# Optimization experiments

Measured on AMD Instinct MI355X. Metric: run time of the kernel, lower is better.

The kernel has to match this reference:

```python
import jax, jax.numpy as jnp
import numpy as np


def gcn_conv(h, W, b, src, dst):
    # PyG GCNConv: h @ W, add self-loops, symmetric deg^-1/2 normalization,
    # scatter-add messages from src to dst, then add bias.
    n = h.shape[0]
    h = h @ W                                   # [N, out]
    loop = jnp.arange(n, dtype=src.dtype)
    row = jnp.concatenate([src, loop])          # message sources
    col = jnp.concatenate([dst, loop])          # aggregation targets
    deg = jax.ops.segment_sum(jnp.ones_like(col, dtype=h.dtype), col, num_segments=n)
    dinv = jnp.where(deg > 0, jax.lax.rsqrt(deg), 0.0)
    norm = dinv[row] * dinv[col]                # [E+N]
    out = jax.ops.segment_sum(h[row] * norm[:, None], col, num_segments=n)
    return out + b


def setup_inputs() -> dict:
    key = jax.random.key(0)
    ks = jax.random.split(key, 12)
    N, E = 50000, 800000
    in_dim, hid, out_dim = 768, 256, 128
    x = jax.random.normal(ks[0], (N, in_dim), dtype=jnp.float32)
    edge_index = jax.random.randint(ks[1], (2, E), 0, N, dtype=jnp.int64)

    def lin(k, fan_in, fan_out):
        bound = 1.0 / np.sqrt(fan_in)
        kw, kb = jax.random.split(k)
        W = jax.random.uniform(kw, (fan_in, fan_out), jnp.float32, -bound, bound)
        b = jax.random.uniform(kb, (fan_out,), jnp.float32, -bound, bound)
        return W, b

    W1, b1 = lin(ks[2], in_dim, hid)
    Wg1, bg1 = lin(ks[3], hid, hid)
    Wg2, bg2 = lin(ks[4], hid, hid)
    W2, b2 = lin(ks[5], hid, out_dim)
    Wc, bc = lin(ks[6], out_dim, 2)
    return {
        "x": x, "edge_index": edge_index,
        "W1": W1, "b1": b1, "Wg1": Wg1, "bg1": bg1,
        "Wg2": Wg2, "bg2": bg2, "W2": W2, "b2": b2,
        "Wc": Wc, "bc": bc, "batch_size": 1024,
    }


def reference(x, edge_index, W1, b1, Wg1, bg1, Wg2, bg2, W2, b2, Wc, bc, batch_size):
    src, dst = edge_index[0], edge_index[1]
    h = jax.nn.relu(x @ W1 + b1)                # linear_relu1
    h = gcn_conv(h, Wg1, bg1, src, dst)         # text1
    # dropout is identity in eval mode
    h = gcn_conv(h, Wg2, bg2, src, dst)         # text2
    h = jax.nn.relu(h @ W2 + b2)                # linear_relu2
    logits = h @ Wc + bc                        # classifier
    return logits[:batch_size]
```

## Files before the change

### kernel.cpp

```cpp
#include <hip/hip_runtime.h>
#include <hip/hip_bf16.h>
#include <cstdint>
#include <cstddef>
#include <type_traits>

typedef _Float16 half8 __attribute__((ext_vector_type(8)));
typedef _Float16 half4v __attribute__((ext_vector_type(4)));
typedef float float4v __attribute__((ext_vector_type(4)));


__global__ void k_zero_int(int* __restrict__ p, int n) {
  int i = blockIdx.x * blockDim.x + threadIdx.x;
  if (i < n) p[i] = 0;
}

__global__ void k_count(const int* __restrict__ dst, int* __restrict__ cnt, int E) {
  int e = blockIdx.x * blockDim.x + threadIdx.x;
  if (e < E) atomicAdd(&cnt[dst[e]], 1);
}

__global__ __launch_bounds__(1024) void k_scan_local(const int* __restrict__ cnt,
                                                     int* __restrict__ rowp,
                                                     int* __restrict__ bsum, int n) {
  __shared__ int sm[1024];
  int tid = threadIdx.x;
  int i = blockIdx.x * 1024 + tid;
  int v = (i < n) ? cnt[i] : 0;
  sm[tid] = v;
  __syncthreads();
  for (int off = 1; off < 1024; off <<= 1) {
    int t = (tid >= off) ? sm[tid - off] : 0;
    __syncthreads();
    sm[tid] += t;
    __syncthreads();
  }
  if (i < n) rowp[i] = sm[tid] - v;
  if (tid == 1023) bsum[blockIdx.x] = sm[1023];
}

__global__ __launch_bounds__(1024) void k_scan_sums(int* __restrict__ bsum, int nb) {
  __shared__ int sm[1024];
  int tid = threadIdx.x;
  int v = (tid < nb) ? bsum[tid] : 0;
  sm[tid] = v;
  __syncthreads();
  for (int off = 1; off < 1024; off <<= 1) {
    int t = (tid >= off) ? sm[tid - off] : 0;
    __syncthreads();
    sm[tid] += t;
    __syncthreads();
  }
  if (tid < nb) bsum[tid] = sm[tid] - v;
}

__global__ void k_finalize(int* __restrict__ rowp, const int* __restrict__ bsum,
                           const int* __restrict__ cnt, int* __restrict__ cursor,
                           float* __restrict__ dinv, int n, int E) {
  int i = blockIdx.x * blockDim.x + threadIdx.x;
  if (i < n) {
    int v = rowp[i] + bsum[i >> 10];
    rowp[i] = v;
    cursor[i] = v;
    dinv[i] = rsqrtf((float)(cnt[i] + 1));
  }
  if (i == 0) rowp[n] = E;
}

__global__ void k_fill(const int* __restrict__ src, const int* __restrict__ dst,
                       int* __restrict__ cursor, int* __restrict__ csr_src, int E) {
  int e = blockIdx.x * blockDim.x + threadIdx.x;
  if (e < E) {
    int pos = atomicAdd(&cursor[dst[e]], 1);
    csr_src[pos] = src[e];
  }
}


__global__ void k_w_convert_all(const float* __restrict__ W1, const float* __restrict__ Wg1,
                                const float* __restrict__ Wg2, _Float16* __restrict__ W1t,
                                _Float16* __restrict__ Wg1t, _Float16* __restrict__ Wg2t,
                                int in_dim, int hid) {
  int idx = blockIdx.x * blockDim.x + threadIdx.x;
  int n1 = in_dim * hid;
  int n2 = hid * hid;
  if (idx < n1) {
    int n = idx / in_dim, k = idx - n * in_dim;
    W1t[idx] = (_Float16)W1[(size_t)k * hid + n];
  } else if (idx < n1 + n2) {
    int i2 = idx - n1;
    int n = i2 / hid, k = i2 - n * hid;
    Wg1t[i2] = (_Float16)Wg1[(size_t)k * hid + n];
  } else if (idx < n1 + 2 * n2) {
    int i2 = idx - n1 - n2;
    int n = i2 / hid, k = i2 - n * hid;
    Wg2t[i2] = (_Float16)Wg2[(size_t)k * hid + n];
  }
}


#define LDSS 40

template <typename AT>
__device__ __forceinline__ half8 load_row_h8(const AT* __restrict__ p, bool ok) {
  half8 v = {};
  if (ok) {
    if constexpr (std::is_same_v<AT, float>) {
      float4 f0 = *(const float4*)p;
      float4 f1 = *(const float4*)(p + 4);
      v[0] = (_Float16)f0.x; v[1] = (_Float16)f0.y;
      v[2] = (_Float16)f0.z; v[3] = (_Float16)f0.w;
      v[4] = (_Float16)f1.x; v[5] = (_Float16)f1.y;
      v[6] = (_Float16)f1.z; v[7] = (_Float16)f1.w;
    } else {
      v = *(const half8*)p;
    }
  }
  return v;
}

template <typename AT, int RELU, int BIAS>
__global__ __launch_bounds__(256, 3) void k_gemm_mfma(const AT* __restrict__ A,
                                                      const _Float16* __restrict__ Bt,
                                                      const float* __restrict__ bias,
                                                      _Float16* __restrict__ out,
                                                      int M, int N, int K) {
  __shared__ _Float16 Asm[2][128 * LDSS];
  __shared__ _Float16 Bsm[2][128 * LDSS];
  const int tid = threadIdx.x;
  const int bm = blockIdx.y * 128;
  const int bn = blockIdx.x * 128;
  const int wave = tid >> 6;
  const int wm = (wave >> 1) * 64;
  const int wn = (wave & 1) * 64;
  const int quad = (tid & 63) >> 4;
  const int l15 = tid & 15;
  const int r0 = tid >> 2;
  const int c0 = (tid & 3) * 8;

  const int gr0 = bm + r0, gr1 = bm + r0 + 64;
  const bool ok0 = gr0 < M, ok1 = gr1 < M;
  const AT* Ap0 = A + (size_t)gr0 * K + c0;
  const AT* Ap1 = A + (size_t)gr1 * K + c0;
  const _Float16* Bp0 = Bt + (size_t)(bn + r0) * K + c0;
  const _Float16* Bp1 = Bt + (size_t)(bn + r0 + 64) * K + c0;

  _Float16* As0 = &Asm[0][0] + r0 * LDSS + c0;
  _Float16* As1 = &Asm[0][0] + (r0 + 64) * LDSS + c0;
  _Float16* Bs0 = &Bsm[0][0] + r0 * LDSS + c0;
  _Float16* Bs1 = &Bsm[0][0] + (r0 + 64) * LDSS + c0;
  const int bufstep = 128 * LDSS;

  float4v acc[4][4];
#pragma unroll
  for (int i = 0; i < 4; ++i)
#pragma unroll
    for (int j = 0; j < 4; ++j) acc[i][j] = (float4v){0.f, 0.f, 0.f, 0.f};

  half8 pa0 = load_row_h8<AT>(Ap0, ok0);
  half8 pa1 = load_row_h8<AT>(Ap1, ok1);
  half8 pb0 = *(const half8*)Bp0;
  half8 pb1 = *(const half8*)Bp1;
  *(half8*)As0 = pa0;
  *(half8*)As1 = pa1;
  *(half8*)Bs0 = pb0;
  *(half8*)Bs1 = pb1;

  const int nk = K >> 5;
  int buf = 0;
  for (int kt = 0; kt < nk; ++kt) {
    __syncthreads();
    if (kt + 1 < nk) {
      int k0 = (kt + 1) << 5;
      pa0 = load_row_h8<AT>(Ap0 + k0, ok0);
      pa1 = load_row_h8<AT>(Ap1 + k0, ok1);
      pb0 = *(const half8*)(Bp0 + k0);
      pb1 = *(const half8*)(Bp1 + k0);
    }
    const _Float16* Ab = &Asm[0][0] + buf * bufstep;
    const _Float16* Bb = &Bsm[0][0] + buf * bufstep;
    half8 af[4], bf[4];
#pragma unroll
    for (int i = 0; i < 4; ++i)
      af[i] = *(const half8*)(Ab + (wm + i * 16 + l15) * LDSS + quad * 8);
#pragma unroll
    for (int j = 0; j < 4; ++j)
      bf[j] = *(const half8*)(Bb + (wn + j * 16 + l15) * LDSS + quad * 8);
#pragma unroll
    for (int i = 0; i < 4; ++i)
#pragma unroll
      for (int j = 0; j < 4; ++j)
        acc[i][j] = __builtin_amdgcn_mfma_f32_16x16x32_f16(af[i], bf[j], acc[i][j], 0, 0, 0);
    if (kt + 1 < nk) {
      int nbuf = buf ^ 1;
      *(half8*)(As0 + nbuf * bufstep) = pa0;
      *(half8*)(As1 + nbuf * bufstep) = pa1;
      *(half8*)(Bs0 + nbuf * bufstep) = pb0;
      *(half8*)(Bs1 + nbuf * bufstep) = pb1;
    }
    buf ^= 1;
  }

#pragma unroll
  for (int j = 0; j < 4; ++j) {
    int c = bn + wn + j * 16 + l15;
    float bv = BIAS ? bias[c] : 0.f;
#pragma unroll
    for (int i = 0; i < 4; ++i) {
      int rbase = bm + wm + i * 16 + quad * 4;
      float4v a = acc[i][j];
#pragma unroll
      for (int reg = 0; reg < 4; ++reg) {
        int r = rbase + reg;
        if (r < M) {
          float v = a[reg] + bv;
          if (RELU) v = fmaxf(v, 0.f);
          out[(size_t)r * N + c] = (_Float16)v;
        }
      }
    }
  }
}


template <int RELU, int BIAS>
__global__ __launch_bounds__(256) void k_gemm(const float* __restrict__ A,
                                              const float* __restrict__ B,
                                              const float* __restrict__ bias,
                                              float* __restrict__ C,
                                              int M, int N, int K) {
  __shared__ float As[16][68];
  __shared__ float Bs[16][68];
  const int bm = blockIdx.y * 64;
  const int bn = blockIdx.x * 64;
  const int tid = threadIdx.x;
  const int tr = (tid >> 4) << 2;
  const int tc = (tid & 15) << 2;
  const int lm  = tid >> 2;
  const int lk  = (tid & 3) << 2;
  const int lk2 = tid >> 4;
  const int ln  = (tid & 15) << 2;
  const bool arow_ok = (bm + lm) < M;
  const float* Aptr = A + (size_t)(bm + lm) * K + lk;
  const float* Bptr = B + (size_t)lk2 * N + bn + ln;
  float acc[4][4] = {};
  for (int k0 = 0; k0 < K; k0 += 16) {
    float4 a4 = make_float4(0.f, 0.f, 0.f, 0.f);
    if (arow_ok) a4 = *(const float4*)(Aptr + k0);
    float4 b4 = *(const float4*)(Bptr + (size_t)k0 * N);
    As[lk + 0][lm] = a4.x;
    As[lk + 1][lm] = a4.y;
    As[lk + 2][lm] = a4.z;
    As[lk + 3][lm] = a4.w;
    *(float4*)&Bs[lk2][ln] = b4;
    __syncthreads();
#pragma unroll
    for (int k = 0; k < 16; ++k) {
      float4 av = *(const float4*)&As[k][tr];
      float4 bv = *(const float4*)&Bs[k][tc];
      float a[4] = {av.x, av.y, av.z, av.w};
      float b[4] = {bv.x, bv.y, bv.z, bv.w};
#pragma unroll
      for (int i = 0; i < 4; ++i)
#pragma unroll
        for (int j = 0; j < 4; ++j) acc[i][j] += a[i] * b[j];
    }
    __syncthreads();
  }
  float bias_v[4] = {0.f, 0.f, 0.f, 0.f};
  if (BIAS) {
    float4 bb = *(const float4*)(bias + bn + tc);
    bias_v[0] = bb.x; bias_v[1] = bb.y; bias_v[2] = bb.z; bias_v[3] = bb.w;
  }
#pragma unroll
  for (int i = 0; i < 4; ++i) {
    int r = bm + tr + i;
    if (r < M) {
      float4 o;
      o.x = acc[i][0] + bias_v[0];
      o.y = acc[i][1] + bias_v[1];
      o.z = acc[i][2] + bias_v[2];
      o.w = acc[i][3] + bias_v[3];
      if (RELU) {
        o.x = fmaxf(o.x, 0.f); o.y = fmaxf(o.y, 0.f);
        o.z = fmaxf(o.z, 0.f); o.w = fmaxf(o.w, 0.f);
      }
      *(float4*)&C[(size_t)r * N + bn + tc] = o;
    }
  }
}


template <typename OT>
__global__ __launch_bounds__(256) void k_agg(const _Float16* __restrict__ t,
                                             const int* __restrict__ row_ptr,
                                             const int* __restrict__ csr_src,
                                             const float* __restrict__ dinv,
                                             const float* __restrict__ bias,
                                             OT* __restrict__ out, int n_nodes) {
  int w = (int)((blockIdx.x * 256 + threadIdx.x) >> 6);
  int lane = threadIdx.x & 63;
  if (w >= n_nodes) return;
  float di = dinv[w];
  half4v v = *(const half4v*)(t + (size_t)w * 256 + lane * 4);
  float sw = di * di;
  float ax = (float)v[0] * sw, ay = (float)v[1] * sw, az = (float)v[2] * sw, aw = (float)v[3] * sw;
  int e0 = row_ptr[w], e1 = row_ptr[w + 1];
  for (int e = e0; e < e1; ++e) {
    int s = csr_src[e];
    float wgt = dinv[s] * di;
    half4v u = *(const half4v*)(t + (size_t)s * 256 + lane * 4);
    ax += (float)u[0] * wgt; ay += (float)u[1] * wgt;
    az += (float)u[2] * wgt; aw += (float)u[3] * wgt;
  }
  const float4 b = ((const float4*)bias)[lane];
  if constexpr (std::is_same_v<OT, float>) {
    float4 o;
    o.x = ax + b.x; o.y = ay + b.y; o.z = az + b.z; o.w = aw + b.w;
    ((float4*)(out + (size_t)w * 256))[lane] = o;
  } else {
    half4v o;
    o[0] = (_Float16)(ax + b.x); o[1] = (_Float16)(ay + b.y);
    o[2] = (_Float16)(az + b.z); o[3] = (_Float16)(aw + b.w);
    *(half4v*)(out + (size_t)w * 256 + lane * 4) = o;
  }
}


__global__ __launch_bounds__(256) void k_cls(const float* __restrict__ h,
                                             const float* __restrict__ Wc,
                                             const float* __restrict__ bc,
                                             float* __restrict__ out, int M, int K) {
  __shared__ float w[512];
  for (int i = threadIdx.x; i < 2 * K; i += 256) w[i] = Wc[i];
  __syncthreads();
  int i = blockIdx.x * 256 + threadIdx.x;
  if (i >= M) return;
  float a0 = bc[0], a1 = bc[1];
  const float* hr = h + (size_t)i * K;
  for (int k = 0; k < K; ++k) {
    float a = hr[k];
    a0 += a * w[2 * k];
    a1 += a * w[2 * k + 1];
  }
  out[2 * i] = a0;
  out[2 * i + 1] = a1;
}


extern "C" void kernel_launch(void* const* d_in, const int* in_sizes, int n_in,
                              void* d_out, int out_size, void* d_ws, size_t ws_size,
                              hipStream_t stream) {
  const float* x   = (const float*)d_in[0];
  const int*   ei  = (const int*)d_in[1];
  const float* W1  = (const float*)d_in[2];
  const float* b1  = (const float*)d_in[3];
  const float* Wg1 = (const float*)d_in[4];
  const float* bg1 = (const float*)d_in[5];
  const float* Wg2 = (const float*)d_in[6];
  const float* bg2 = (const float*)d_in[7];
  const float* W2  = (const float*)d_in[8];
  const float* b2  = (const float*)d_in[9];
  const float* Wc  = (const float*)d_in[10];
  const float* bc  = (const float*)d_in[11];
  float* out = (float*)d_out;

  const int hid     = in_sizes[3];
  const int in_dim  = in_sizes[2] / hid;
  const int out_dim = in_sizes[9];
  const int N       = in_sizes[0] / in_dim;
  const int E       = in_sizes[1] / 2;
  const int Batch   = out_size / 2;

  const int* srcI = ei;
  const int* dstI = ei + E;

  char* ws = (char*)d_ws;
  size_t off = 0;
  auto alloc = [&](size_t bytes) -> void* {
    void* p = ws + off;
    off = (off + bytes + 255) & ~(size_t)255;
    return p;
  };
  _Float16* h0h  = (_Float16*)alloc((size_t)N * hid * 2);
  _Float16* t1h  = (_Float16*)alloc((size_t)N * hid * 2);
  _Float16* h1h  = (_Float16*)alloc((size_t)N * hid * 2);
  _Float16* t2h  = (_Float16*)alloc((size_t)N * hid * 2);
  _Float16* W1t  = (_Float16*)alloc((size_t)in_dim * hid * 2);
  _Float16* Wg1t = (_Float16*)alloc((size_t)hid * hid * 2);
  _Float16* Wg2t = (_Float16*)alloc((size_t)hid * hid * 2);
  float* agg2    = (float*)alloc((size_t)Batch * hid * 4);
  float* h3      = (float*)alloc((size_t)Batch * out_dim * 4);
  float* dinv    = (float*)alloc((size_t)N * 4);
  int*   cnt     = (int*)alloc((size_t)N * 4);
  int*   rowp    = (int*)alloc((size_t)(N + 1) * 4);
  int*   bsum    = (int*)alloc((size_t)1024 * 4);
  int*   cursor  = (int*)alloc((size_t)N * 4);
  int*   csrs    = (int*)alloc((size_t)E * 4);
  (void)ws_size; (void)n_in;

  dim3 blk(256);
  const int nb = (N + 1023) / 1024;

  k_zero_int<<<(N + 255) / 256, blk, 0, stream>>>(cnt, N);
  k_count<<<(E + 255) / 256, blk, 0, stream>>>(dstI, cnt, E);
  k_scan_local<<<nb, 1024, 0, stream>>>(cnt, rowp, bsum, N);
  k_scan_sums<<<1, 1024, 0, stream>>>(bsum, nb);
  k_finalize<<<(N + 255) / 256, blk, 0, stream>>>(rowp, bsum, cnt, cursor, dinv, N, E);
  k_fill<<<(E + 255) / 256, blk, 0, stream>>>(srcI, dstI, cursor, csrs, E);

  {
    int total = in_dim * hid + 2 * hid * hid;
    k_w_convert_all<<<(total + 255) / 256, blk, 0, stream>>>(W1, Wg1, Wg2, W1t, Wg1t, Wg2t, in_dim, hid);
  }

  dim3 gemm_grid(hid / 128, (N + 127) / 128);
  k_gemm_mfma<float, 1, 1><<<gemm_grid, blk, 0, stream>>>(x, W1t, b1, h0h, N, hid, in_dim);
  k_gemm_mfma<_Float16, 0, 0><<<gemm_grid, blk, 0, stream>>>(h0h, Wg1t, nullptr, t1h, N, hid, hid);
  k_agg<_Float16><<<(N + 3) / 4, blk, 0, stream>>>(t1h, rowp, csrs, dinv, bg1, h1h, N);
  k_gemm_mfma<_Float16, 0, 0><<<gemm_grid, blk, 0, stream>>>(h1h, Wg2t, nullptr, t2h, N, hid, hid);
  k_agg<float><<<(Batch + 3) / 4, blk, 0, stream>>>(t2h, rowp, csrs, dinv, bg2, agg2, Batch);
  k_gemm<1, 1><<<dim3(out_dim / 64, (Batch + 63) / 64), blk, 0, stream>>>(agg2, W2, b2, h3, Batch, out_dim, hid);
  k_cls<<<(Batch + 255) / 256, blk, 0, stream>>>(h3, Wc, bc, out, Batch, out_dim);
}
```

Baseline: 551.1 us.

## Fold source-degree scaling into GEMM epilogue, unroll aggregation, shrink GEMM M-tile

The GCN GEMMs now multiply each output row by dinv[row], so the aggregation kernel no longer gathers dinv[src] per edge. It sums the prescaled rows and applies dinv[dst] once at the end, with the edge loop unrolled by four to keep more gathers in flight. The MFMA GEMM tile drops from 128 to 64 rows, with the occupancy hint raised to 4 blocks per CU. The smaller tile gives more blocks but less operand reuse per block, and the prescaled values are rounded to fp16 before accumulation.

```diff
diff --git a/kernel.cpp b/kernel.cpp
--- a/kernel.cpp
+++ b/kernel.cpp
@@ -118,52 +118,55 @@
   return v;
 }
 
-template <typename AT, int RELU, int BIAS>
-__global__ __launch_bounds__(256, 3) void k_gemm_mfma(const AT* __restrict__ A,
+template <typename AT, int RELU, int BIAS, int SCALE>
+__global__ __launch_bounds__(256, 4) void k_gemm_mfma(const AT* __restrict__ A,
                                                       const _Float16* __restrict__ Bt,
                                                       const float* __restrict__ bias,
+                                                      const float* __restrict__ rowscale,
                                                       _Float16* __restrict__ out,
                                                       int M, int N, int K) {
-  __shared__ _Float16 Asm[2][128 * LDSS];
+  __shared__ _Float16 Asm[2][64 * LDSS];
   __shared__ _Float16 Bsm[2][128 * LDSS];
   const int tid = threadIdx.x;
-  const int bm = blockIdx.y * 128;
+  const int bm = blockIdx.y * 64;
   const int bn = blockIdx.x * 128;
   const int wave = tid >> 6;
-  const int wm = (wave >> 1) * 64;
+  const int wm = (wave >> 1) * 32;
   const int wn = (wave & 1) * 64;
   const int quad = (tid & 63) >> 4;
   const int l15 = tid & 15;
-  const int r0 = tid >> 2;
-  const int c0 = (tid & 3) * 8;
-
-  const int gr0 = bm + r0, gr1 = bm + r0 + 64;
-  const bool ok0 = gr0 < M, ok1 = gr1 < M;
-  const AT* Ap0 = A + (size_t)gr0 * K + c0;
-  const AT* Ap1 = A + (size_t)gr1 * K + c0;
-  const _Float16* Bp0 = Bt + (size_t)(bn + r0) * K + c0;
-  const _Float16* Bp1 = Bt + (size_t)(bn + r0 + 64) * K + c0;
-
-  _Float16* As0 = &Asm[0][0] + r0 * LDSS + c0;
-  _Float16* As1 = &Asm[0][0] + (r0 + 64) * LDSS + c0;
-  _Float16* Bs0 = &Bsm[0][0] + r0 * LDSS + c0;
-  _Float16* Bs1 = &Bsm[0][0] + (r0 + 64) * LDSS + c0;
-  const int bufstep = 128 * LDSS;
-
-  float4v acc[4][4];
-#pragma unroll
-  for (int i = 0; i < 4; ++i)
+
+  const int ar = tid >> 2;
+  const int ac = (tid & 3) * 8;
+  const int br0 = tid >> 1;
+
+  const int gra = bm + ar;
+  const bool oka = gra < M;
+  const AT* Apt = A + (size_t)gra * K + ac;
+  const int br_0 = tid >> 2, bc_0 = (tid & 3) * 8;
+  const int br_1 = (tid + 256) >> 2, bc_1 = ((tid + 256) & 3) * 8;
+  const _Float16* Bp0 = Bt + (size_t)(bn + br_0) * K + bc_0;
+  const _Float16* Bp1 = Bt + (size_t)(bn + br_1) * K + bc_1;
+
+  _Float16* AsW = &Asm[0][0] + ar * LDSS + ac;
+  _Float16* BsW0 = &Bsm[0][0] + br_0 * LDSS + bc_0;
+  _Float16* BsW1 = &Bsm[0][0] + br_1 * LDSS + bc_1;
+  const int abufstep = 64 * LDSS;
+  const int bbufstep = 128 * LDSS;
+  (void)br0;
+
+  float4v acc[2][4];
+#pragma unroll
+  for (int i = 0; i < 2; ++i)
 #pragma unroll
     for (int j = 0; j < 4; ++j) acc[i][j] = (float4v){0.f, 0.f, 0.f, 0.f};
 
-  half8 pa0 = load_row_h8<AT>(Ap0, ok0);
-  half8 pa1 = load_row_h8<AT>(Ap1, ok1);
+  half8 pa = load_row_h8<AT>(Apt, oka);
   half8 pb0 = *(const half8*)Bp0;
   half8 pb1 = *(const half8*)Bp1;
-  *(half8*)As0 = pa0;
-  *(half8*)As1 = pa1;
-  *(half8*)Bs0 = pb0;
-  *(half8*)Bs1 = pb1;
+  *(half8*)AsW = pa;
+  *(half8*)BsW0 = pb0;
+  *(half8*)BsW1 = pb1;
 
   const int nk = K >> 5;
   int buf = 0;
@@ -171,31 +174,29 @@
     __syncthreads();
     if (kt + 1 < nk) {
       int k0 = (kt + 1) << 5;
-      pa0 = load_row_h8<AT>(Ap0 + k0, ok0);
-      pa1 = load_row_h8<AT>(Ap1 + k0, ok1);
+      pa = load_row_h8<AT>(Apt + k0, oka);
       pb0 = *(const half8*)(Bp0 + k0);
       pb1 = *(const half8*)(Bp1 + k0);
     }
-    const _Float16* Ab = &Asm[0][0] + buf * bufstep;
-    const _Float16* Bb = &Bsm[0][0] + buf * bufstep;
-    half8 af[4], bf[4];
-#pragma unroll
-    for (int i = 0; i < 4; ++i)
+    const _Float16* Ab = &Asm[0][0] + buf * abufstep;
+    const _Float16* Bb = &Bsm[0][0] + buf * bbufstep;
+    half8 af[2], bf[4];
+#pragma unroll
+    for (int i = 0; i < 2; ++i)
       af[i] = *(const half8*)(Ab + (wm + i * 16 + l15) * LDSS + quad * 8);
 #pragma unroll
     for (int j = 0; j < 4; ++j)
       bf[j] = *(const half8*)(Bb + (wn + j * 16 + l15) * LDSS + quad * 8);
 #pragma unroll
-    for (int i = 0; i < 4; ++i)
+    for (int i = 0; i < 2; ++i)
 #pragma unroll
       for (int j = 0; j < 4; ++j)
         acc[i][j] = __builtin_amdgcn_mfma_f32_16x16x32_f16(af[i], bf[j], acc[i][j], 0, 0, 0);
     if (kt + 1 < nk) {
       int nbuf = buf ^ 1;
-      *(half8*)(As0 + nbuf * bufstep) = pa0;
-      *(half8*)(As1 + nbuf * bufstep) = pa1;
-      *(half8*)(Bs0 + nbuf * bufstep) = pb0;
-      *(half8*)(Bs1 + nbuf * bufstep) = pb1;
+      *(half8*)(AsW + nbuf * abufstep) = pa;
+      *(half8*)(BsW0 + nbuf * bbufstep) = pb0;
+      *(half8*)(BsW1 + nbuf * bbufstep) = pb1;
     }
     buf ^= 1;
   }
@@ -205,7 +206,7 @@
     int c = bn + wn + j * 16 + l15;
     float bv = BIAS ? bias[c] : 0.f;
 #pragma unroll
-    for (int i = 0; i < 4; ++i) {
+    for (int i = 0; i < 2; ++i) {
       int rbase = bm + wm + i * 16 + quad * 4;
       float4v a = acc[i][j];
 #pragma unroll
@@ -214,6 +215,7 @@
         if (r < M) {
           float v = a[reg] + bv;
           if (RELU) v = fmaxf(v, 0.f);
+          if (SCALE) v *= rowscale[r];
           out[(size_t)r * N + c] = (_Float16)v;
         }
       }
@@ -302,25 +304,38 @@
   if (w >= n_nodes) return;
   float di = dinv[w];
   half4v v = *(const half4v*)(t + (size_t)w * 256 + lane * 4);
-  float sw = di * di;
-  float ax = (float)v[0] * sw, ay = (float)v[1] * sw, az = (float)v[2] * sw, aw = (float)v[3] * sw;
+  float ax = (float)v[0], ay = (float)v[1], az = (float)v[2], aw = (float)v[3];
   int e0 = row_ptr[w], e1 = row_ptr[w + 1];
-  for (int e = e0; e < e1; ++e) {
+  int e = e0;
+  for (; e + 4 <= e1; e += 4) {
+    int s0 = csr_src[e];
+    int s1 = csr_src[e + 1];
+    int s2 = csr_src[e + 2];
+    int s3 = csr_src[e + 3];
+    half4v u0 = *(const half4v*)(t + (size_t)s0 * 256 + lane * 4);
+    half4v u1 = *(const half4v*)(t + (size_t)s1 * 256 + lane * 4);
+    half4v u2 = *(const half4v*)(t + (size_t)s2 * 256 + lane * 4);
+    half4v u3 = *(const half4v*)(t + (size_t)s3 * 256 + lane * 4);
+    ax += (float)u0[0] + (float)u1[0] + (float)u2[0] + (float)u3[0];
+    ay += (float)u0[1] + (float)u1[1] + (float)u2[1] + (float)u3[1];
+    az += (float)u0[2] + (float)u1[2] + (float)u2[2] + (float)u3[2];
+    aw += (float)u0[3] + (float)u1[3] + (float)u2[3] + (float)u3[3];
+  }
+  for (; e < e1; ++e) {
     int s = csr_src[e];
-    float wgt = dinv[s] * di;
     half4v u = *(const half4v*)(t + (size_t)s * 256 + lane * 4);
-    ax += (float)u[0] * wgt; ay += (float)u[1] * wgt;
-    az += (float)u[2] * wgt; aw += (float)u[3] * wgt;
+    ax += (float)u[0]; ay += (float)u[1]; az += (float)u[2]; aw += (float)u[3];
   }
   const float4 b = ((const float4*)bias)[lane];
   if constexpr (std::is_same_v<OT, float>) {
     float4 o;
-    o.x = ax + b.x; o.y = ay + b.y; o.z = az + b.z; o.w = aw + b.w;
+    o.x = ax * di + b.x; o.y = ay * di + b.y;
+    o.z = az * di + b.z; o.w = aw * di + b.w;
     ((float4*)(out + (size_t)w * 256))[lane] = o;
   } else {
     half4v o;
-    o[0] = (_Float16)(ax + b.x); o[1] = (_Float16)(ay + b.y);
-    o[2] = (_Float16)(az + b.z); o[3] = (_Float16)(aw + b.w);
+    o[0] = (_Float16)(ax * di + b.x); o[1] = (_Float16)(ay * di + b.y);
+    o[2] = (_Float16)(az * di + b.z); o[3] = (_Float16)(aw * di + b.w);
     *(half4v*)(out + (size_t)w * 256 + lane * 4) = o;
   }
 }
@@ -413,11 +428,11 @@
     k_w_convert_all<<<(total + 255) / 256, blk, 0, stream>>>(W1, Wg1, Wg2, W1t, Wg1t, Wg2t, in_dim, hid);
   }
 
-  dim3 gemm_grid(hid / 128, (N + 127) / 128);
-  k_gemm_mfma<float, 1, 1><<<gemm_grid, blk, 0, stream>>>(x, W1t, b1, h0h, N, hid, in_dim);
-  k_gemm_mfma<_Float16, 0, 0><<<gemm_grid, blk, 0, stream>>>(h0h, Wg1t, nullptr, t1h, N, hid, hid);
+  dim3 gemm_grid(hid / 128, (N + 63) / 64);
+  k_gemm_mfma<float, 1, 1, 0><<<gemm_grid, blk, 0, stream>>>(x, W1t, b1, nullptr, h0h, N, hid, in_dim);
+  k_gemm_mfma<_Float16, 0, 0, 1><<<gemm_grid, blk, 0, stream>>>(h0h, Wg1t, nullptr, dinv, t1h, N, hid, hid);
   k_agg<_Float16><<<(N + 3) / 4, blk, 0, stream>>>(t1h, rowp, csrs, dinv, bg1, h1h, N);
-  k_gemm_mfma<_Float16, 0, 0><<<gemm_grid, blk, 0, stream>>>(h1h, Wg2t, nullptr, t2h, N, hid, hid);
+  k_gemm_mfma<_Float16, 0, 0, 1><<<gemm_grid, blk, 0, stream>>>(h1h, Wg2t, nullptr, dinv, t2h, N, hid, hid);
   k_agg<float><<<(Batch + 3) / 4, blk, 0, stream>>>(t2h, rowp, csrs, dinv, bg2, agg2, Batch);
   k_gemm<1, 1><<<dim3(out_dim / 64, (Batch + 63) / 64), blk, 0, stream>>>(agg2, W2, b2, h3, Batch, out_dim, hid);
   k_cls<<<(Batch + 255) / 256, blk, 0, stream>>>(h3, Wc, bc, out, Batch, out_dim);
```

New measurement: 538.4 us. 1.02x faster.
